# Kernel optimization log

Hardware: AMD Instinct MI355X
Metric: run time of the kernel (lower is better)

The kernel has to match this reference:

```python
import jax, jax.numpy as jnp
import numpy as np

B, A, V, H, F, ND, NC, NE, NL = 4096, 768, 2048, 512, 1024, 16, 2, 8, 3


def setup_inputs() -> dict:
    key = jax.random.key(0)
    ks = jax.random.split(key, 16)

    def g(k, shape, fan_in):
        return jax.random.normal(k, shape, jnp.float32) * (1.0 / np.sqrt(fan_in))

    return {
        "audio": jax.random.normal(ks[0], (B, A), jnp.float32),
        "video": jax.random.normal(ks[1], (B, V), jnp.float32),
        "disease_idx": jax.random.randint(ks[2], (B,), 0, ND),
        "Wa": g(ks[3], (A, H), A), "ba": jnp.zeros((H,), jnp.float32),
        "Wv": g(ks[4], (V, H), V), "bv": jnp.zeros((H,), jnp.float32),
        "Pa": g(ks[5], (H, F), H), "Cva": g(ks[6], (H, F), H),
        "Pv": g(ks[7], (H, F), H), "Cav": g(ks[8], (H, F), H),
        "Wproj": g(ks[9], (2 * F, F), 2 * F), "bproj": jnp.zeros((F,), jnp.float32),
        "Wf": g(ks[10], (NL, F, F), F), "bf": jnp.zeros((NL, F), jnp.float32),
        "Wc1": g(ks[11], (ND, F, 256), F), "bc1": jnp.zeros((ND, 256), jnp.float32),
        "Wc2": g(ks[12], (ND, 256, NC), 256), "bc2": jnp.zeros((ND, NC), jnp.float32),
        "We1": g(ks[13], (H, 128), H), "be1": jnp.zeros((128,), jnp.float32),
        "We2": g(ks[14], (128, NE), 128), "be2": jnp.zeros((NE,), jnp.float32),
    }


def reference(audio, video, disease_idx, Wa, ba, Wv, bv, Pa, Cva, Pv, Cav,
              Wproj, bproj, Wf, bf, Wc1, bc1, Wc2, bc2, We1, be1, We2, be2):
    # Audio / video feature encoders (stand-ins for AudioModel / VideoModel)
    af = jax.nn.relu(audio @ Wa + ba)            # (B, H)
    vf = jax.nn.relu(video @ Wv + bv)            # (B, H)

    # Cross-modal mixing block: each stream attends to (mixes in) the other
    attended_audio = af @ Pa + vf @ Cva          # (B, F)
    attended_video = vf @ Pv + af @ Cav          # (B, F)

    # Concat fusion; 2F != F so the on-the-fly fusion projection is applied
    fused = jnp.concatenate([attended_audio, attended_video], axis=1)  # (B, 2F)
    fused = fused @ Wproj + bproj                # (B, F)

    # Fusion MLP: NL x (Linear -> ReLU), trailing Dropout stripped (inference)
    for i in range(NL):
        fused = jax.nn.relu(fused @ Wf[i] + bf[i])

    # Disease-indexed per-sample head dispatch.
    # Reference computes all heads densely then gathers by disease_idx —
    # identical math to the per-sample Python loop in the torch code.
    h_all = jax.nn.relu(jnp.einsum("bf,nfh->bnh", fused, Wc1) + bc1)   # (B, ND, 256)
    l_all = jnp.einsum("bnh,nhc->bnc", h_all, Wc2) + bc2               # (B, ND, NC)
    logits = jnp.take_along_axis(l_all, disease_idx[:, None, None], axis=1)[:, 0, :]  # (B, NC)

    # Auxiliary emotion head on video features
    emotion_logits = jax.nn.relu(vf @ We1 + be1) @ We2 + be2            # (B, NE)

    return logits, af, vf, fused, emotion_logits
```

## Files before the change

### kernel.cpp

```cpp
#include <hip/hip_runtime.h>
#include <hip/hip_bf16.h>
#include <stdint.h>


typedef __attribute__((ext_vector_type(8))) short bf16x8;
typedef __attribute__((ext_vector_type(4))) float f32x4;

__device__ inline short f2b(float f) {
  union { float f; uint32_t u; } a; a.f = f;
  uint32_t r = a.u + 0x7fffu + ((a.u >> 16) & 1u);
  return (short)(r >> 16);
}
__device__ inline float b2f(short s) {
  union { uint32_t u; float f; } a; a.u = ((uint32_t)(uint16_t)s) << 16;
  return a.f;
}
__device__ inline void gload_lds16(const void* g, void* l) {
  __builtin_amdgcn_global_load_lds(
      (const __attribute__((address_space(1))) uint32_t*)g,
      (__attribute__((address_space(3))) uint32_t*)l, 16, 0, 0);
}
template<int N> __device__ __forceinline__ void waitv() {
  asm volatile("s_waitcnt vmcnt(%0)" :: "n"(N) : "memory");
}

__global__ __launch_bounds__(256)
void prep_k(const float* __restrict__ Wa, const float* __restrict__ Wv,
            const float* __restrict__ Wproj, const float* __restrict__ Wf,
            const float* __restrict__ Wc1, const float* __restrict__ We1,
            const float* __restrict__ Pa, const float* __restrict__ Cva,
            const float* __restrict__ Cav, const float* __restrict__ Pv,
            const float* __restrict__ audio, const float* __restrict__ video,
            const int* __restrict__ didx,
            short* __restrict__ WaT, short* __restrict__ WvT,
            short* __restrict__ WprojT, short* __restrict__ WfT,
            short* __restrict__ Wc1T, short* __restrict__ We1T,
            short* __restrict__ Watt, short* __restrict__ a_bf,
            short* __restrict__ v_bf,
            int* __restrict__ perm, int* __restrict__ bstart,
            int* __restrict__ bmap) {
  __shared__ short t[64][66];
  __shared__ int cnt[16], base[17], curp[16];
  int b = blockIdx.x;
  const int tid = threadIdx.x;

  if (b == 6000) {
    if (tid < 16) cnt[tid] = 0;
    __syncthreads();
    for (int r = tid; r < 4096; r += 256) atomicAdd(&cnt[didx[r]], 1);
    __syncthreads();
    if (tid == 0) {
      int s = 0;
      for (int d = 0; d < 16; ++d) { base[d] = s; s += cnt[d]; }
      base[16] = s;
      int nb = 0;
      for (int d = 0; d < 16; ++d) {
        int nblk = (cnt[d] + 63) >> 6;
        for (int i = 0; i < nblk; ++i) bmap[nb++] = (d << 8) | i;
      }
      bstart[17] = nb;
    }
    __syncthreads();
    if (tid < 16) curp[tid] = base[tid];
    if (tid < 17) bstart[tid] = base[tid];
    __syncthreads();
    for (int r = tid; r < 4096; r += 256) {
      int p = atomicAdd(&curp[didx[r]], 1);
      perm[p] = r;
    }
    return;
  }
  if (b >= 3184) {
    const float* in; short* out;
    if (b < 3952) { b -= 3184; in = audio; out = a_bf; }
    else          { b -= 3952; in = video; out = v_bf; }
    const long base_ = (long)b * 4096;
#pragma unroll
    for (int p = 0; p < 4; ++p) {
      const long i = base_ + ((p * 256 + tid) << 2);
      float4 v = *(const float4*)(in + i);
      short4 o; o.x = f2b(v.x); o.y = f2b(v.y); o.z = f2b(v.z); o.w = f2b(v.w);
      *(short4*)(out + i) = o;
    }
    return;
  }
  if (b >= 2672) {
    b -= 2672;
    const int q = b >> 7, r4 = (b & 127) << 2;
    const float* src; int rowoff, coloff;
    if (q == 0)      { src = Pa;  rowoff = 0;   coloff = 0; }
    else if (q == 1) { src = Cav; rowoff = 0;   coloff = 1024; }
    else if (q == 2) { src = Cva; rowoff = 512; coloff = 0; }
    else             { src = Pv;  rowoff = 512; coloff = 1024; }
#pragma unroll
    for (int p = 0; p < 4; ++p) {
      const int item = p * 256 + tid;
      const int h = r4 + (item >> 8), j = (item & 255) << 2;
      float4 v = *(const float4*)(src + (long)h * 1024 + j);
      short4 o; o.x = f2b(v.x); o.y = f2b(v.y); o.z = f2b(v.z); o.w = f2b(v.w);
      *(short4*)(Watt + (long)(rowoff + h) * 2048 + coloff + j) = o;
    }
    return;
  }

  const float* in; short* out; int N, ldout, nnb;
  if (b < 96)        { in = Wa;    out = WaT;    N = 512;  ldout = 768;  nnb = 8; }
  else if (b < 352)  { b -= 96;  in = Wv;    out = WvT;    N = 512;  ldout = 2048; nnb = 8; }
  else if (b < 864)  { b -= 352; in = Wproj; out = WprojT; N = 1024; ldout = 2048; nnb = 16; }
  else if (b < 1632) { b -= 864; int z = b >> 8; b &= 255;
                       in = Wf + (long)z * 1048576; out = WfT + (long)z * 1048576;
                       N = 1024; ldout = 1024; nnb = 16; }
  else if (b < 2656) { b -= 1632; int z = b >> 6; b &= 63;
                       in = Wc1 + (long)z * 262144; out = Wc1T + (long)z * 262144;
                       N = 256; ldout = 1024; nnb = 4; }
  else               { b -= 2656; in = We1; out = We1T; N = 128; ldout = 512; nnb = 2; }
  const int n0 = (b % nnb) << 6, k0 = (b / nnb) << 6;

#pragma unroll
  for (int p = 0; p < 4; ++p) {
    const int item = p * 256 + tid;
    const int row = item >> 4, c4 = (item & 15) << 2;
    float4 v = *(const float4*)(in + (long)(k0 + row) * N + n0 + c4);
    short4 o; o.x = f2b(v.x); o.y = f2b(v.y); o.z = f2b(v.z); o.w = f2b(v.w);
    *(short4*)&t[row][c4] = o;
  }
  __syncthreads();
#pragma unroll
  for (int p = 0; p < 4; ++p) {
    const int item = p * 256 + tid;
    const int kg4 = item & 15, n = item >> 4;
    short4 o;
    o.x = t[4 * kg4 + 0][n]; o.y = t[4 * kg4 + 1][n];
    o.z = t[4 * kg4 + 2][n]; o.w = t[4 * kg4 + 3][n];
    *(short4*)(out + (long)(n0 + n) * ldout + k0 + 4 * kg4) = o;
  }
}

template<int BM, int BN, bool RELU, bool HASF32>
__device__ __forceinline__
void gemm_body(const short* __restrict__ A, const short* __restrict__ BT,
               const float* __restrict__ bias,
               short* __restrict__ Cb, int ldcb,
               float* __restrict__ Cf, int ldcf,
               int K, int lda, int ldbt, int m0, int n0,
               short* lds) {
  constexpr int MR = BM / 32, NR = BN / 32;
  constexpr int S = MR + NR;
  constexpr int BUF = (BM + BN) * 64;
  const int tid = threadIdx.x;
  const int w = tid >> 6, l = tid & 63;
  const int wr = w >> 1, wc = w & 1;
  const int lr = l & 15, lk = (l >> 4) << 3;

  f32x4 acc[MR][NR];
#pragma unroll
  for (int m = 0; m < MR; ++m)
#pragma unroll
    for (int n = 0; n < NR; ++n) acc[m][n] = (f32x4)0.f;

  const int r_ = tid >> 3;
  const int kc_ = (((tid & 7) ^ (r_ & 7)) << 3);
  const short* Arow = A + (long)(m0 + r_) * lda + kc_;
  const short* Brow = BT + (long)(n0 + r_) * ldbt + kc_;
  const int nk = K >> 6;

  auto stage = [&](int t, int buf) {
    const int kt = t << 6;
    char* sA = (char*)(lds + buf * BUF);
    char* sB = sA + BM * 128;
#pragma unroll
    for (int i = 0; i < MR; ++i)
      gload_lds16(Arow + (long)i * 32 * lda + kt, sA + i * 4096 + w * 1024);
#pragma unroll
    for (int i = 0; i < NR; ++i)
      gload_lds16(Brow + (long)i * 32 * ldbt + kt, sB + i * 4096 + w * 1024);
  };

  stage(0, 0);
  if (nk > 1) stage(1, 1);
  int cur = 0;
  for (int t = 0; t < nk; ++t) {
    __builtin_amdgcn_s_barrier();
    __builtin_amdgcn_sched_barrier(0);
    if (t + 2 < nk) {
      int nxt = cur + 2; if (nxt >= 3) nxt -= 3;
      stage(t + 2, nxt);
      waitv<2 * S>();
    } else if (t + 1 < nk) {
      waitv<S>();
    } else {
      waitv<0>();
    }
    __builtin_amdgcn_s_barrier();
    __builtin_amdgcn_sched_barrier(0);
    const short* sA = lds + cur * BUF;
    const short* sB = sA + BM * 64;
#pragma unroll
    for (int kk = 0; kk < 64; kk += 32) {
      const int cb = (kk + lk) >> 3;
      bf16x8 a[MR], b[NR];
#pragma unroll
      for (int m = 0; m < MR; ++m) {
        const int ra = wr * (BM / 2) + m * 16 + lr;
        a[m] = *(const bf16x8*)&sA[ra * 64 + ((cb ^ (ra & 7)) << 3)];
      }
#pragma unroll
      for (int n = 0; n < NR; ++n) {
        const int rb = wc * (BN / 2) + n * 16 + lr;
        b[n] = *(const bf16x8*)&sB[rb * 64 + ((cb ^ (rb & 7)) << 3)];
      }
#pragma unroll
      for (int m = 0; m < MR; ++m)
#pragma unroll
        for (int n = 0; n < NR; ++n)
          acc[m][n] = __builtin_amdgcn_mfma_f32_16x16x32_bf16(a[m], b[n], acc[m][n], 0, 0, 0);
    }
    __builtin_amdgcn_sched_barrier(0);
    cur = (cur == 2) ? 0 : cur + 1;
  }

  const int lrow = (l >> 4) << 2;
#pragma unroll
  for (int n = 0; n < NR; ++n) {
    const int col = n0 + wc * (BN / 2) + n * 16 + lr;
    const float bz = bias ? bias[col] : 0.f;
#pragma unroll
    for (int m = 0; m < MR; ++m) {
      const int rowb = m0 + wr * (BM / 2) + m * 16 + lrow;
#pragma unroll
      for (int i = 0; i < 4; ++i) {
        float v = acc[m][n][i] + bz;
        if (RELU) v = fmaxf(v, 0.f);
        Cb[(long)(rowb + i) * ldcb + col] = f2b(v);
        if (HASF32) Cf[(long)(rowb + i) * ldcf + col] = v;
      }
    }
  }
}

template<int BM, int BN, bool RELU, bool HASF32>
__global__ __launch_bounds__(256, 2)
void gemm_bt(const short* __restrict__ A, const short* __restrict__ BT,
             const float* __restrict__ bias,
             short* __restrict__ Cb, int ldcb,
             float* __restrict__ Cf, int ldcf,
             int K, int lda, int ldbt) {
  __shared__ short lds[3 * (BM + BN) * 64];
  gemm_body<BM, BN, RELU, HASF32>(A, BT, bias, Cb, ldcb, Cf, ldcf,
                                  K, lda, ldbt, blockIdx.x * BM, blockIdx.y * BN,
                                  lds);
}

__global__ __launch_bounds__(256, 2)
void enc_w2t_k(const short* __restrict__ a_bf, const short* __restrict__ v_bf,
               const short* __restrict__ WaT, const short* __restrict__ WvT,
               const float* __restrict__ ba, const float* __restrict__ bv,
               short* __restrict__ afvf, float* __restrict__ out_af,
               float* __restrict__ out_vf,
               const short* __restrict__ WprojT, const short* __restrict__ Watt_rm,
               short* __restrict__ W2T) {
  __shared__ short lds[3 * (128 + 64) * 64];
  int b = blockIdx.x;
  if (b < 512) {
    const int x = b & 31, y = b >> 5;
    const bool isA = y < 8;
    gemm_body<128, 64, true, true>(
        isA ? a_bf : v_bf, isA ? WaT : WvT, isA ? ba : bv,
        afvf + (isA ? 0 : 512), 1024, isA ? out_af : out_vf, 512,
        isA ? 768 : 2048, isA ? 768 : 2048, isA ? 768 : 2048,
        x << 7, (y & 7) << 6, lds);
  } else {
    b -= 512;
    gemm_body<64, 32, false, false>(
        WprojT, Watt_rm, nullptr, W2T, 1024, nullptr, 0,
        2048, 2048, 2048, (b & 15) << 6, (b >> 4) << 5, lds);
  }
}

__global__ __launch_bounds__(256, 2)
void g34emo_k(const short* __restrict__ afvf, const short* __restrict__ W2T,
              const float* __restrict__ bproj, short* __restrict__ fusedA,
              const short* __restrict__ We1T, const float* __restrict__ be1,
              short* __restrict__ e1_bf) {
  __shared__ short lds[3 * (128 + 64) * 64];
  int b = blockIdx.x;
  if (b < 512) {
    gemm_body<128, 64, false, false>(
        afvf, W2T, bproj, fusedA, 1024, nullptr, 0,
        1024, 1024, 1024, (b & 31) << 7, (b >> 5) << 6, lds);
  } else {
    b -= 512;
    gemm_body<64, 32, true, false>(
        afvf + 512, We1T, be1, e1_bf, 128, nullptr, 0,
        512, 1024, 512, (b & 63) << 6, (b >> 6) << 5, lds);
  }
}

__global__ __launch_bounds__(256, 2)
void head_gemm(const short* __restrict__ fused, const short* __restrict__ Wc1T,
               const float* __restrict__ bc1, const int* __restrict__ perm,
               const int* __restrict__ bstart, const int* __restrict__ bmap,
               short* __restrict__ h) {
  const int nb = bstart[17];
  if ((int)blockIdx.x >= nb) return;
  const int me = bmap[blockIdx.x];
  const int d = me >> 8, rt = me & 0xff;
  const int b0 = bstart[d], cnt = bstart[d + 1] - b0;
  const int t0 = rt << 6;
  const int c0 = blockIdx.y << 6;
  __shared__ short lds[3 * 128 * 64];
  const int tid = threadIdx.x, w = tid >> 6, l = tid & 63;
  const int wr = w >> 1, wc = w & 1;
  const int lr = l & 15, lk = (l >> 4) << 3;
  const short* BT = Wc1T + (long)d * (256 * 1024) + (long)c0 * 1024;

  f32x4 acc[2][2];
#pragma unroll
  for (int m = 0; m < 2; ++m)
#pragma unroll
    for (int n = 0; n < 2; ++n) acc[m][n] = (f32x4)0.f;

  const int r_ = tid >> 3;
  const int kc_ = (((tid & 7) ^ (r_ & 7)) << 3);
  int gr0 = (t0 + r_      < cnt) ? perm[b0 + t0 + r_]      : perm[b0];
  int gr1 = (t0 + r_ + 32 < cnt) ? perm[b0 + t0 + r_ + 32] : perm[b0];
  const short* A0 = fused + (long)gr0 * 1024 + kc_;
  const short* A1 = fused + (long)gr1 * 1024 + kc_;
  const short* Brow = BT + (long)r_ * 1024 + kc_;

  auto stage = [&](int t, int buf) {
    const int kt = t << 6;
    char* sA = (char*)lds + buf * 16384;
    char* sB = sA + 8192;
    gload_lds16(A0 + kt, sA + w * 1024);
    gload_lds16(A1 + kt, sA + 4096 + w * 1024);
    gload_lds16(Brow + kt, sB + w * 1024);
    gload_lds16(Brow + 32 * 1024 + kt, sB + 4096 + w * 1024);
  };

  stage(0, 0);
  stage(1, 1);
  int cur = 0;
  for (int t = 0; t < 16; ++t) {
    __builtin_amdgcn_s_barrier();
    __builtin_amdgcn_sched_barrier(0);
    if (t + 2 < 16) {
      int nxt = cur + 2; if (nxt >= 3) nxt -= 3;
      stage(t + 2, nxt);
      waitv<8>();
    } else if (t + 1 < 16) {
      waitv<4>();
    } else {
      waitv<0>();
    }
    __builtin_amdgcn_s_barrier();
    __builtin_amdgcn_sched_barrier(0);
    const short* sA = lds + cur * 8192;
    const short* sB = sA + 4096;
#pragma unroll
    for (int kk = 0; kk < 64; kk += 32) {
      const int cb = (kk + lk) >> 3;
      bf16x8 a[2], b[2];
#pragma unroll
      for (int m = 0; m < 2; ++m) {
        const int ra = wr * 32 + m * 16 + lr;
        a[m] = *(const bf16x8*)&sA[ra * 64 + ((cb ^ (ra & 7)) << 3)];
      }
#pragma unroll
      for (int n = 0; n < 2; ++n) {
        const int rb = wc * 32 + n * 16 + lr;
        b[n] = *(const bf16x8*)&sB[rb * 64 + ((cb ^ (rb & 7)) << 3)];
      }
#pragma unroll
      for (int m = 0; m < 2; ++m)
#pragma unroll
        for (int n = 0; n < 2; ++n)
          acc[m][n] = __builtin_amdgcn_mfma_f32_16x16x32_bf16(a[m], b[n], acc[m][n], 0, 0, 0);
    }
    __builtin_amdgcn_sched_barrier(0);
    cur = (cur == 2) ? 0 : cur + 1;
  }

#pragma unroll
  for (int m = 0; m < 2; ++m)
#pragma unroll
    for (int i2 = 0; i2 < 4; ++i2) {
      const int lrow = wr * 32 + m * 16 + ((l >> 4) << 2) + i2;
      if (t0 + lrow >= cnt) continue;
      const int gr = perm[b0 + t0 + lrow];
#pragma unroll
      for (int n = 0; n < 2; ++n) {
        const int col = c0 + wc * 32 + n * 16 + lr;
        float v = acc[m][n][i2] + bc1[d * 256 + col];
        v = fmaxf(v, 0.f);
        h[(long)gr * 256 + col] = f2b(v);
      }
    }
}

__global__ __launch_bounds__(256)
void tail_k(const short* __restrict__ h, const float* __restrict__ Wc2,
            const float* __restrict__ bc2, const int* __restrict__ didx,
            const short* __restrict__ e1, const float* __restrict__ We2,
            const float* __restrict__ be2,
            float* __restrict__ out_logits, float* __restrict__ out_emo) {
  const int w = threadIdx.x >> 6, l = threadIdx.x & 63;
  if (blockIdx.x < 1024) {
    const int r = ((int)blockIdx.x << 2) + w;
    const int d = didx[r];
    const short4 hv4 = *(const short4*)(h + (long)r * 256 + (l << 2));
    const float* wr_ = Wc2 + d * 512 + (l << 3);
    const float4 w01 = *(const float4*)wr_;
    const float4 w23 = *(const float4*)(wr_ + 4);
    const float h0 = b2f(hv4.x), h1 = b2f(hv4.y), h2 = b2f(hv4.z), h3 = b2f(hv4.w);
    float a0 = h0 * w01.x + h1 * w01.z + h2 * w23.x + h3 * w23.z;
    float a1 = h0 * w01.y + h1 * w01.w + h2 * w23.y + h3 * w23.w;
#pragma unroll
    for (int off = 32; off > 0; off >>= 1) {
      a0 += __shfl_down(a0, off);
      a1 += __shfl_down(a1, off);
    }
    if (l == 0) {
      out_logits[r * 2 + 0] = a0 + bc2[d * 2 + 0];
      out_logits[r * 2 + 1] = a1 + bc2[d * 2 + 1];
    }
  } else {
    const int r = (((int)blockIdx.x - 1024) << 2) + w;
    const float h0 = b2f(e1[(long)r * 128 + 2 * l]);
    const float h1 = b2f(e1[(long)r * 128 + 2 * l + 1]);
    const float* w0 = We2 + (2 * l) * 8;
    float a[8];
#pragma unroll
    for (int c = 0; c < 8; ++c) a[c] = h0 * w0[c] + h1 * w0[8 + c];
#pragma unroll
    for (int c = 0; c < 8; ++c)
#pragma unroll
      for (int off = 32; off > 0; off >>= 1) a[c] += __shfl_down(a[c], off);
    if (l == 0) {
#pragma unroll
      for (int c = 0; c < 8; ++c) out_emo[r * 8 + c] = a[c] + be2[c];
    }
  }
}

extern "C" void kernel_launch(void* const* d_in, const int* in_sizes, int n_in,
                              void* d_out, int out_size, void* d_ws, size_t ws_size,
                              hipStream_t stream) {
  const float* audio = (const float*)d_in[0];
  const float* video = (const float*)d_in[1];
  const int*   didx  = (const int*)d_in[2];
  const float* Wa    = (const float*)d_in[3];
  const float* ba    = (const float*)d_in[4];
  const float* Wv    = (const float*)d_in[5];
  const float* bv    = (const float*)d_in[6];
  const float* Pa    = (const float*)d_in[7];
  const float* Cva   = (const float*)d_in[8];
  const float* Pv    = (const float*)d_in[9];
  const float* Cav   = (const float*)d_in[10];
  const float* Wproj = (const float*)d_in[11];
  const float* bproj = (const float*)d_in[12];
  const float* Wf    = (const float*)d_in[13];
  const float* bfv   = (const float*)d_in[14];
  const float* Wc1   = (const float*)d_in[15];
  const float* bc1   = (const float*)d_in[16];
  const float* Wc2   = (const float*)d_in[17];
  const float* bc2   = (const float*)d_in[18];
  const float* We1   = (const float*)d_in[19];
  const float* be1   = (const float*)d_in[20];
  const float* We2   = (const float*)d_in[21];
  const float* be2   = (const float*)d_in[22];

  char* ws = (char*)d_ws;
  short* W2T     = (short*)(ws + 0);
  short* WaT     = (short*)(ws + 2097152);
  short* WvT     = (short*)(ws + 2883584);
  short* Watt_rm = (short*)(ws + 4980736);
  short* WprojT  = (short*)(ws + 9175040);
  short* WfT     = (short*)(ws + 13369344);
  short* Wc1T    = (short*)(ws + 19660800);
  short* We1T    = (short*)(ws + 28049408);
  short* afvf    = (short*)(ws + 28180480);
  short* fusedA  = (short*)(ws + 36569088);
  short* fusedB  = (short*)(ws + 44957696);
  short* h_bf    = (short*)(ws + 53346304);
  short* e1_bf   = (short*)(ws + 55443456);
  int*   perm    = (int*)(ws + 56492032);
  int*   bstart  = (int*)(ws + 56508416);
  int*   bmap    = (int*)(ws + 56508544);
  short* a_bf    = (short*)(ws + 56512512);
  short* v_bf    = (short*)(ws + 62803968);

  float* out        = (float*)d_out;
  float* out_logits = out;
  float* out_af     = out + 8192;
  float* out_vf     = out + 2105344;
  float* out_fused  = out + 4202496;
  float* out_emo    = out + 8396800;

  prep_k<<<dim3(6001), dim3(256), 0, stream>>>(
      Wa, Wv, Wproj, Wf, Wc1, We1, Pa, Cva, Cav, Pv, audio, video, didx,
      WaT, WvT, WprojT, WfT, Wc1T, We1T, Watt_rm, a_bf, v_bf,
      perm, bstart, bmap);

  enc_w2t_k<<<dim3(1024), dim3(256), 0, stream>>>(
      a_bf, v_bf, WaT, WvT, ba, bv, afvf, out_af, out_vf,
      WprojT, Watt_rm, W2T);

  g34emo_k<<<dim3(768), dim3(256), 0, stream>>>(
      afvf, W2T, bproj, fusedA, We1T, be1, e1_bf);

  gemm_bt<128, 64, true, false><<<dim3(32, 16), dim3(256), 0, stream>>>(
      fusedA, WfT, bfv, fusedB, 1024, nullptr, 0, 1024, 1024, 1024);
  gemm_bt<128, 64, true, false><<<dim3(32, 16), dim3(256), 0, stream>>>(
      fusedB, WfT + 1048576, bfv + 1024, fusedA, 1024, nullptr, 0, 1024, 1024, 1024);
  gemm_bt<128, 64, true, true><<<dim3(32, 16), dim3(256), 0, stream>>>(
      fusedA, WfT + 2097152, bfv + 2048, fusedB, 1024, out_fused, 1024, 1024, 1024, 1024);

  head_gemm<<<dim3(80, 4), dim3(256), 0, stream>>>(fusedB, Wc1T, bc1, perm, bstart, bmap, h_bf);
  tail_k<<<dim3(2048), dim3(256), 0, stream>>>(
      h_bf, Wc2, bc2, didx, e1_bf, We2, be2, out_logits, out_emo);
}
```

Before: 133.9 us.

## Defer later-stage weight transposes and routing into encoder kernel launch

Moves the transposes of Wf, Wc1 and We1 and the disease-bucketing routine out of the prep kernel and appends them as extra blocks of the encoder GEMM kernel. Those outputs are consumed only by later kernels, so the intent is to shrink the critical-path prep kernel and overlap this bandwidth-bound work with the encoder GEMMs. The risk is that the extra blocks compete with the GEMM blocks for CUs and memory bandwidth, and the routing block may now start late in the grid.

New measurement: 134.7 us. Within noise of the previous version (+0.6%).

```diff
diff --git a/kernel.cpp b/kernel.cpp
--- a/kernel.cpp
+++ b/kernel.cpp
@@ -24,98 +24,11 @@
   asm volatile("s_waitcnt vmcnt(%0)" :: "n"(N) : "memory");
 }
 
-__global__ __launch_bounds__(256)
-void prep_k(const float* __restrict__ Wa, const float* __restrict__ Wv,
-            const float* __restrict__ Wproj, const float* __restrict__ Wf,
-            const float* __restrict__ Wc1, const float* __restrict__ We1,
-            const float* __restrict__ Pa, const float* __restrict__ Cva,
-            const float* __restrict__ Cav, const float* __restrict__ Pv,
-            const float* __restrict__ audio, const float* __restrict__ video,
-            const int* __restrict__ didx,
-            short* __restrict__ WaT, short* __restrict__ WvT,
-            short* __restrict__ WprojT, short* __restrict__ WfT,
-            short* __restrict__ Wc1T, short* __restrict__ We1T,
-            short* __restrict__ Watt, short* __restrict__ a_bf,
-            short* __restrict__ v_bf,
-            int* __restrict__ perm, int* __restrict__ bstart,
-            int* __restrict__ bmap) {
-  __shared__ short t[64][66];
-  __shared__ int cnt[16], base[17], curp[16];
-  int b = blockIdx.x;
+__device__ __forceinline__
+void transpose_tile(const float* __restrict__ in, short* __restrict__ out,
+                    int N, int ldout, int n0, int k0, short* scratch) {
+  short (*t)[66] = (short(*)[66])scratch;
   const int tid = threadIdx.x;
-
-  if (b == 6000) {
-    if (tid < 16) cnt[tid] = 0;
-    __syncthreads();
-    for (int r = tid; r < 4096; r += 256) atomicAdd(&cnt[didx[r]], 1);
-    __syncthreads();
-    if (tid == 0) {
-      int s = 0;
-      for (int d = 0; d < 16; ++d) { base[d] = s; s += cnt[d]; }
-      base[16] = s;
-      int nb = 0;
-      for (int d = 0; d < 16; ++d) {
-        int nblk = (cnt[d] + 63) >> 6;
-        for (int i = 0; i < nblk; ++i) bmap[nb++] = (d << 8) | i;
-      }
-      bstart[17] = nb;
-    }
-    __syncthreads();
-    if (tid < 16) curp[tid] = base[tid];
-    if (tid < 17) bstart[tid] = base[tid];
-    __syncthreads();
-    for (int r = tid; r < 4096; r += 256) {
-      int p = atomicAdd(&curp[didx[r]], 1);
-      perm[p] = r;
-    }
-    return;
-  }
-  if (b >= 3184) {
-    const float* in; short* out;
-    if (b < 3952) { b -= 3184; in = audio; out = a_bf; }
-    else          { b -= 3952; in = video; out = v_bf; }
-    const long base_ = (long)b * 4096;
-#pragma unroll
-    for (int p = 0; p < 4; ++p) {
-      const long i = base_ + ((p * 256 + tid) << 2);
-      float4 v = *(const float4*)(in + i);
-      short4 o; o.x = f2b(v.x); o.y = f2b(v.y); o.z = f2b(v.z); o.w = f2b(v.w);
-      *(short4*)(out + i) = o;
-    }
-    return;
-  }
-  if (b >= 2672) {
-    b -= 2672;
-    const int q = b >> 7, r4 = (b & 127) << 2;
-    const float* src; int rowoff, coloff;
-    if (q == 0)      { src = Pa;  rowoff = 0;   coloff = 0; }
-    else if (q == 1) { src = Cav; rowoff = 0;   coloff = 1024; }
-    else if (q == 2) { src = Cva; rowoff = 512; coloff = 0; }
-    else             { src = Pv;  rowoff = 512; coloff = 1024; }
-#pragma unroll
-    for (int p = 0; p < 4; ++p) {
-      const int item = p * 256 + tid;
-      const int h = r4 + (item >> 8), j = (item & 255) << 2;
-      float4 v = *(const float4*)(src + (long)h * 1024 + j);
-      short4 o; o.x = f2b(v.x); o.y = f2b(v.y); o.z = f2b(v.z); o.w = f2b(v.w);
-      *(short4*)(Watt + (long)(rowoff + h) * 2048 + coloff + j) = o;
-    }
-    return;
-  }
-
-  const float* in; short* out; int N, ldout, nnb;
-  if (b < 96)        { in = Wa;    out = WaT;    N = 512;  ldout = 768;  nnb = 8; }
-  else if (b < 352)  { b -= 96;  in = Wv;    out = WvT;    N = 512;  ldout = 2048; nnb = 8; }
-  else if (b < 864)  { b -= 352; in = Wproj; out = WprojT; N = 1024; ldout = 2048; nnb = 16; }
-  else if (b < 1632) { b -= 864; int z = b >> 8; b &= 255;
-                       in = Wf + (long)z * 1048576; out = WfT + (long)z * 1048576;
-                       N = 1024; ldout = 1024; nnb = 16; }
-  else if (b < 2656) { b -= 1632; int z = b >> 6; b &= 63;
-                       in = Wc1 + (long)z * 262144; out = Wc1T + (long)z * 262144;
-                       N = 256; ldout = 1024; nnb = 4; }
-  else               { b -= 2656; in = We1; out = We1T; N = 128; ldout = 512; nnb = 2; }
-  const int n0 = (b % nnb) << 6, k0 = (b / nnb) << 6;
-
 #pragma unroll
   for (int p = 0; p < 4; ++p) {
     const int item = p * 256 + tid;
@@ -134,6 +47,58 @@
     o.z = t[4 * kg4 + 2][n]; o.w = t[4 * kg4 + 3][n];
     *(short4*)(out + (long)(n0 + n) * ldout + k0 + 4 * kg4) = o;
   }
+}
+
+__global__ __launch_bounds__(256)
+void prep_k(const float* __restrict__ Wa, const float* __restrict__ Wv,
+            const float* __restrict__ Wproj,
+            const float* __restrict__ Pa, const float* __restrict__ Cva,
+            const float* __restrict__ Cav, const float* __restrict__ Pv,
+            const float* __restrict__ audio, const float* __restrict__ video,
+            short* __restrict__ WaT, short* __restrict__ WvT,
+            short* __restrict__ WprojT, short* __restrict__ Watt,
+            short* __restrict__ a_bf, short* __restrict__ v_bf) {
+  __shared__ short t[64 * 66];
+  int b = blockIdx.x;
+  const int tid = threadIdx.x;
+
+  if (b >= 1376) {
+    const float* in; short* out;
+    if (b < 2144) { b -= 1376; in = audio; out = a_bf; }
+    else          { b -= 2144; in = video; out = v_bf; }
+    const long base_ = (long)b * 4096;
+#pragma unroll
+    for (int p = 0; p < 4; ++p) {
+      const long i = base_ + ((p * 256 + tid) << 2);
+      float4 v = *(const float4*)(in + i);
+      short4 o; o.x = f2b(v.x); o.y = f2b(v.y); o.z = f2b(v.z); o.w = f2b(v.w);
+      *(short4*)(out + i) = o;
+    }
+    return;
+  }
+  if (b >= 864) {
+    b -= 864;
+    const int q = b >> 7, r4 = (b & 127) << 2;
+    const float* src; int rowoff, coloff;
+    if (q == 0)      { src = Pa;  rowoff = 0;   coloff = 0; }
+    else if (q == 1) { src = Cav; rowoff = 0;   coloff = 1024; }
+    else if (q == 2) { src = Cva; rowoff = 512; coloff = 0; }
+    else             { src = Pv;  rowoff = 512; coloff = 1024; }
+#pragma unroll
+    for (int p = 0; p < 4; ++p) {
+      const int item = p * 256 + tid;
+      const int h = r4 + (item >> 8), j = (item & 255) << 2;
+      float4 v = *(const float4*)(src + (long)h * 1024 + j);
+      short4 o; o.x = f2b(v.x); o.y = f2b(v.y); o.z = f2b(v.z); o.w = f2b(v.w);
+      *(short4*)(Watt + (long)(rowoff + h) * 2048 + coloff + j) = o;
+    }
+    return;
+  }
+  const float* in; short* out; int N, ldout, nnb;
+  if (b < 96)       { in = Wa;    out = WaT;    N = 512;  ldout = 768;  nnb = 8; }
+  else if (b < 352) { b -= 96;  in = Wv;    out = WvT;    N = 512;  ldout = 2048; nnb = 8; }
+  else              { b -= 352; in = Wproj; out = WprojT; N = 1024; ldout = 2048; nnb = 16; }
+  transpose_tile(in, out, N, ldout, (b % nnb) << 6, (b / nnb) << 6, t);
 }
 
 template<int BM, int BN, bool RELU, bool HASF32>
@@ -258,9 +223,16 @@
                short* __restrict__ afvf, float* __restrict__ out_af,
                float* __restrict__ out_vf,
                const short* __restrict__ WprojT, const short* __restrict__ Watt_rm,
-               short* __restrict__ W2T) {
+               short* __restrict__ W2T,
+               const float* __restrict__ Wf, const float* __restrict__ Wc1,
+               const float* __restrict__ We1,
+               short* __restrict__ WfT, short* __restrict__ Wc1T,
+               short* __restrict__ We1T,
+               const int* __restrict__ didx, int* __restrict__ perm,
+               int* __restrict__ bstart, int* __restrict__ bmap) {
   __shared__ short lds[3 * (128 + 64) * 64];
   int b = blockIdx.x;
+  const int tid = threadIdx.x;
   if (b < 512) {
     const int x = b & 31, y = b >> 5;
     const bool isA = y < 8;
@@ -269,11 +241,47 @@
         afvf + (isA ? 0 : 512), 1024, isA ? out_af : out_vf, 512,
         isA ? 768 : 2048, isA ? 768 : 2048, isA ? 768 : 2048,
         x << 7, (y & 7) << 6, lds);
-  } else {
+  } else if (b < 1024) {
     b -= 512;
     gemm_body<64, 32, false, false>(
         WprojT, Watt_rm, nullptr, W2T, 1024, nullptr, 0,
         2048, 2048, 2048, (b & 15) << 6, (b >> 4) << 5, lds);
+  } else if (b < 2832) {
+    b -= 1024;
+    const float* in; short* out; int N, ldout, nnb;
+    if (b < 768)       { int z = b >> 8; b &= 255;
+                         in = Wf + (long)z * 1048576; out = WfT + (long)z * 1048576;
+                         N = 1024; ldout = 1024; nnb = 16; }
+    else if (b < 1792) { b -= 768; int z = b >> 6; b &= 63;
+                         in = Wc1 + (long)z * 262144; out = Wc1T + (long)z * 262144;
+                         N = 256; ldout = 1024; nnb = 4; }
+    else               { b -= 1792; in = We1; out = We1T; N = 128; ldout = 512; nnb = 2; }
+    transpose_tile(in, out, N, ldout, (b % nnb) << 6, (b / nnb) << 6, lds);
+  } else {
+    int* cnt = (int*)lds; int* base = cnt + 16; int* curp = base + 17;
+    if (tid < 16) cnt[tid] = 0;
+    __syncthreads();
+    for (int r = tid; r < 4096; r += 256) atomicAdd(&cnt[didx[r]], 1);
+    __syncthreads();
+    if (tid == 0) {
+      int s = 0;
+      for (int d = 0; d < 16; ++d) { base[d] = s; s += cnt[d]; }
+      base[16] = s;
+      int nb = 0;
+      for (int d = 0; d < 16; ++d) {
+        int nblk = (cnt[d] + 63) >> 6;
+        for (int i = 0; i < nblk; ++i) bmap[nb++] = (d << 8) | i;
+      }
+      bstart[17] = nb;
+    }
+    __syncthreads();
+    if (tid < 16) curp[tid] = base[tid];
+    if (tid < 17) bstart[tid] = base[tid];
+    __syncthreads();
+    for (int r = tid; r < 4096; r += 256) {
+      int p = atomicAdd(&curp[didx[r]], 1);
+      perm[p] = r;
+    }
   }
 }
 
@@ -497,14 +505,15 @@
   float* out_fused  = out + 4202496;
   float* out_emo    = out + 8396800;
 
-  prep_k<<<dim3(6001), dim3(256), 0, stream>>>(
-      Wa, Wv, Wproj, Wf, Wc1, We1, Pa, Cva, Cav, Pv, audio, video, didx,
-      WaT, WvT, WprojT, WfT, Wc1T, We1T, Watt_rm, a_bf, v_bf,
-      perm, bstart, bmap);
-
-  enc_w2t_k<<<dim3(1024), dim3(256), 0, stream>>>(
+  prep_k<<<dim3(4192), dim3(256), 0, stream>>>(
+      Wa, Wv, Wproj, Pa, Cva, Cav, Pv, audio, video,
+      WaT, WvT, WprojT, Watt_rm, a_bf, v_bf);
+
+  enc_w2t_k<<<dim3(2833), dim3(256), 0, stream>>>(
       a_bf, v_bf, WaT, WvT, ba, bv, afvf, out_af, out_vf,
-      WprojT, Watt_rm, W2T);
+      WprojT, Watt_rm, W2T,
+      Wf, Wc1, We1, WfT, Wc1T, We1T,
+      didx, perm, bstart, bmap);
 
   g34emo_k<<<dim3(768), dim3(256), 0, stream>>>(
       afvf, W2T, bproj, fusedA, We1T, be1, e1_bf);
```
